# Performance work log

Hardware: AMD Instinct MI355X
Metric: run time of the kernel (lower is better)

## Reference

```python
import jax, jax.numpy as jnp
import numpy as np

B, S, H = 4, 2048, 1024
NUM_HEADS = 16
HEAD_DIM = H // NUM_HEADS


def setup_inputs() -> dict:
    key = jax.random.key(0)
    ks = jax.random.split(key, 11)
    s = 0.02
    return {
        "query": jax.random.normal(ks[0], (B, S, H), dtype=jnp.float32),
        "key_in": jax.random.normal(ks[1], (B, S, H), dtype=jnp.float32),
        "value": jax.random.normal(ks[2], (B, S, H), dtype=jnp.float32),
        "Wq": jax.random.normal(ks[3], (H, H), dtype=jnp.float32) * s,
        "bq": jnp.zeros((H,), dtype=jnp.float32),
        "Wk": jax.random.normal(ks[4], (H, H), dtype=jnp.float32) * s,
        "bk": jnp.zeros((H,), dtype=jnp.float32),
        "Wv": jax.random.normal(ks[5], (HEAD_DIM, H), dtype=jnp.float32) * s,
        "bv": jnp.zeros((HEAD_DIM,), dtype=jnp.float32),
        "Wo": jax.random.normal(ks[6], (H, HEAD_DIM), dtype=jnp.float32) * s,
        "bo": jnp.zeros((H,), dtype=jnp.float32),
    }


def reference(query, key_in, value, Wq, bq, Wk, bk, Wv, bv, Wo, bo):
    scale = HEAD_DIM ** -0.5
    # Linear projections (torch Linear: x @ W.T + b)
    Q = (query @ Wq.T + bq).reshape(B, S, NUM_HEADS, HEAD_DIM).transpose(0, 2, 1, 3)  # [B,h,S,d]
    K = (key_in @ Wk.T + bk).reshape(B, S, NUM_HEADS, HEAD_DIM).transpose(0, 2, 1, 3)  # [B,h,S,d]
    V = value @ Wv.T + bv  # shared single V: [B,S,d]
    attn_scores = jnp.einsum("bhqd,bhkd->bhqk", Q, K) * scale  # [B,h,S,S]
    attn_weights = jax.nn.softmax(attn_scores, axis=-1)
    # dropout is identity at inference
    avg_attn = attn_weights.mean(axis=1)  # head-averaged weights [B,S,S]
    attn_out = jnp.einsum("bqk,bkd->bqd", avg_attn, V)  # [B,S,d]
    output = attn_out @ Wo.T + bo  # [B,S,H]
    return output, avg_attn
```

## Files before the change

kernel.cpp:

```cpp
#include <hip/hip_runtime.h>
#include <hip/hip_bf16.h>


typedef float f32x4 __attribute__((ext_vector_type(4)));
typedef short s16x8 __attribute__((ext_vector_type(8)));

#define DEVI static __device__ __forceinline__
#define MFMA16(a, b, c) __builtin_amdgcn_mfma_f32_16x16x32_bf16(a, b, c, 0, 0, 0)

DEVI unsigned short f2bf(float f) {
  union { float f; unsigned u; } v; v.f = f;
  return (unsigned short)((v.u + 0x7fffu + ((v.u >> 16) & 1u)) >> 16);
}

DEVI s16x8 pack2(f32x4 lo, f32x4 hi) {
  s16x8 r;
  r[0] = (short)f2bf(lo[0]); r[1] = (short)f2bf(lo[1]);
  r[2] = (short)f2bf(lo[2]); r[3] = (short)f2bf(lo[3]);
  r[4] = (short)f2bf(hi[0]); r[5] = (short)f2bf(hi[1]);
  r[6] = (short)f2bf(hi[2]); r[7] = (short)f2bf(hi[3]);
  return r;
}

DEVI float fast_exp2(float x) {
#if __has_builtin(__builtin_amdgcn_exp2f)
  return __builtin_amdgcn_exp2f(x);
#else
  return exp2f(x);
#endif
}

__global__ __launch_bounds__(256, 2) void proj_qk(
    const float* __restrict__ q_in, const float* __restrict__ k_in,
    const float* __restrict__ Wq, const float* __restrict__ Wk,
    const float* __restrict__ bq, const float* __restrict__ bk,
    unsigned short* __restrict__ Qb, unsigned short* __restrict__ Kb) {
  const float* A = blockIdx.z ? k_in : q_in;
  const float* Bw = blockIdx.z ? Wk : Wq;
  const float* bias = blockIdx.z ? bk : bq;
  unsigned short* C = blockIdx.z ? Kb : Qb;

  __shared__ short As[128][32];
  __shared__ short Bs[128][32];

  const int t = threadIdx.x;
  const int lane = t & 63, wid = t >> 6;
  const int wm = wid >> 1, wn = wid & 1;
  const int fr = lane & 15, g = lane >> 4;
  const int m0 = blockIdx.x * 128, n0 = blockIdx.y * 128;

  const int sr = t >> 1, sc = (t & 1) * 16;
  const float* Ap = A + (size_t)(m0 + sr) * 1024 + sc;
  const float* Bp = Bw + (size_t)(n0 + sr) * 1024 + sc;

  f32x4 acc[4][4];
#pragma unroll
  for (int i = 0; i < 4; ++i)
#pragma unroll
    for (int j = 0; j < 4; ++j) acc[i][j] = (f32x4){0.f, 0.f, 0.f, 0.f};

  for (int kt = 0; kt < 32; ++kt) {
    const f32x4 ar0 = *(const f32x4*)(Ap + 0), ar1 = *(const f32x4*)(Ap + 4),
                ar2 = *(const f32x4*)(Ap + 8), ar3 = *(const f32x4*)(Ap + 12);
    const f32x4 br0 = *(const f32x4*)(Bp + 0), br1 = *(const f32x4*)(Bp + 4),
                br2 = *(const f32x4*)(Bp + 8), br3 = *(const f32x4*)(Bp + 12);
    Ap += 32; Bp += 32;
    __syncthreads();
    *(s16x8*)&As[sr][sc] = pack2(ar0, ar1);
    *(s16x8*)&As[sr][sc + 8] = pack2(ar2, ar3);
    *(s16x8*)&Bs[sr][sc] = pack2(br0, br1);
    *(s16x8*)&Bs[sr][sc + 8] = pack2(br2, br3);
    __syncthreads();

    s16x8 af[4], bf[4];
#pragma unroll
    for (int mt = 0; mt < 4; ++mt) af[mt] = *(const s16x8*)&As[wm * 64 + mt * 16 + fr][g * 8];
#pragma unroll
    for (int nt = 0; nt < 4; ++nt) bf[nt] = *(const s16x8*)&Bs[wn * 64 + nt * 16 + fr][g * 8];
#pragma unroll
    for (int mt = 0; mt < 4; ++mt)
#pragma unroll
      for (int nt = 0; nt < 4; ++nt)
        acc[mt][nt] = MFMA16(af[mt], bf[nt], acc[mt][nt]);
  }

#pragma unroll
  for (int nt = 0; nt < 4; ++nt) {
    const int col = n0 + wn * 64 + nt * 16 + fr;
    const float bb = bias[col];
#pragma unroll
    for (int mt = 0; mt < 4; ++mt) {
      const int row = m0 + wm * 64 + mt * 16 + g * 4;
#pragma unroll
      for (int r = 0; r < 4; ++r)
        C[(size_t)(row + r) * 1024 + col] = f2bf(acc[mt][nt][r] + bb);
    }
  }
}

__global__ __launch_bounds__(256, 2) void proj_v(
    const float* __restrict__ val, const float* __restrict__ Wv,
    const float* __restrict__ bv, unsigned short* __restrict__ Vt) {
  __shared__ short As[64][32];
  __shared__ short Bs[64][32];
  const int t = threadIdx.x, lane = t & 63, w = t >> 6;
  const int fr = lane & 15, g = lane >> 4;
  const int m0 = blockIdx.x * 64;
  const int sr = t >> 2, sc = (t & 3) * 8;
  const float* Ap = val + (size_t)(m0 + sr) * 1024 + sc;
  const float* Bp = Wv + (size_t)sr * 1024 + sc;

  f32x4 acc[4];
#pragma unroll
  for (int i = 0; i < 4; ++i) acc[i] = (f32x4){0.f, 0.f, 0.f, 0.f};

  for (int kt = 0; kt < 32; ++kt) {
    const f32x4 a0 = *(const f32x4*)Ap, a1 = *(const f32x4*)(Ap + 4);
    const f32x4 b0 = *(const f32x4*)Bp, b1 = *(const f32x4*)(Bp + 4);
    Ap += 32; Bp += 32;
    __syncthreads();
    *(s16x8*)&As[sr][sc] = pack2(a0, a1);
    *(s16x8*)&Bs[sr][sc] = pack2(b0, b1);
    __syncthreads();
    const s16x8 a = *(const s16x8*)&As[w * 16 + fr][g * 8];
#pragma unroll
    for (int nt = 0; nt < 4; ++nt) {
      const s16x8 b = *(const s16x8*)&Bs[nt * 16 + fr][g * 8];
      acc[nt] = MFMA16(a, b, acc[nt]);
    }
  }
#pragma unroll
  for (int nt = 0; nt < 4; ++nt) {
    const int d = nt * 16 + fr;
    const float bb = bv[d];
#pragma unroll
    for (int r = 0; r < 4; ++r) {
      const int srow = m0 + w * 16 + g * 4 + r;
      Vt[((size_t)(srow >> 11) * 64 + d) * 2048 + (srow & 2047)] = f2bf(acc[nt][r] + bb);
    }
  }
}

__global__ __launch_bounds__(512, 2) void attn_avg(
    const unsigned short* __restrict__ Qb, const unsigned short* __restrict__ Kb,
    float* __restrict__ avg_out) {
  __shared__ short Qs[16 * 1024];
  __shared__ float redm[16][8];
  __shared__ float redl[16][8];

  const int t = threadIdx.x, lane = t & 63, w = t >> 6;
  const int fr = lane & 15, g = lane >> 4;
  int bx = blockIdx.x;
  bx = (bx & 7) * 64 + (bx >> 3);
  const int b = bx >> 7, q0 = (bx & 127) << 4;

  const unsigned short* Qrow = Qb + (size_t)(b * 2048 + q0) * 1024;
#pragma unroll
  for (int j = 0; j < 4; ++j) {
    const int c = t + 512 * j;
    *(s16x8*)(Qs + c * 8) = *(const s16x8*)(Qrow + c * 8);
  }
  __syncthreads();

  float avg[16][4];
#pragma unroll
  for (int kt = 0; kt < 16; ++kt)
#pragma unroll
    for (int r = 0; r < 4; ++r) avg[kt][r] = 0.f;

  const float cs = 0.125f * 1.44269504088896340736f;
  const unsigned short* Kbase = Kb + (size_t)(b * 2048 + w * 256) * 1024;

  for (int h = 0; h < 16; ++h) {
    const s16x8 a0 = *(const s16x8*)&Qs[fr * 1024 + h * 64 + g * 8];
    const s16x8 a1 = *(const s16x8*)&Qs[fr * 1024 + h * 64 + 32 + g * 8];
    float s[16][4];
    float mx[4] = {-3.0e38f, -3.0e38f, -3.0e38f, -3.0e38f};
#pragma unroll
    for (int kt = 0; kt < 16; ++kt) {
      const unsigned short* kp = Kbase + (size_t)(kt * 16 + fr) * 1024 + h * 64 + g * 8;
      const s16x8 b0 = *(const s16x8*)kp;
      const s16x8 b1 = *(const s16x8*)(kp + 32);
      f32x4 sc = (f32x4){0.f, 0.f, 0.f, 0.f};
      sc = MFMA16(a0, b0, sc);
      sc = MFMA16(a1, b1, sc);
#pragma unroll
      for (int r = 0; r < 4; ++r) { s[kt][r] = sc[r]; mx[r] = fmaxf(mx[r], sc[r]); }
    }
#pragma unroll
    for (int d = 1; d < 16; d <<= 1)
#pragma unroll
      for (int r = 0; r < 4; ++r) mx[r] = fmaxf(mx[r], __shfl_xor(mx[r], d));
    if (fr == 0) {
#pragma unroll
      for (int r = 0; r < 4; ++r) redm[g * 4 + r][w] = mx[r];
    }
    __syncthreads();
    float mc[4], lsum[4];
#pragma unroll
    for (int r = 0; r < 4; ++r) {
      const f32x4 p0 = *(const f32x4*)&redm[g * 4 + r][0];
      const f32x4 p1 = *(const f32x4*)&redm[g * 4 + r][4];
      const float m8 = fmaxf(fmaxf(fmaxf(p0[0], p0[1]), fmaxf(p0[2], p0[3])),
                             fmaxf(fmaxf(p1[0], p1[1]), fmaxf(p1[2], p1[3])));
      mc[r] = m8 * cs;
      lsum[r] = 0.f;
    }
#pragma unroll
    for (int kt = 0; kt < 16; ++kt)
#pragma unroll
      for (int r = 0; r < 4; ++r) {
        const float e = fast_exp2(s[kt][r] * cs - mc[r]);
        s[kt][r] = e;
        lsum[r] += e;
      }
#pragma unroll
    for (int d = 1; d < 16; d <<= 1)
#pragma unroll
      for (int r = 0; r < 4; ++r) lsum[r] += __shfl_xor(lsum[r], d);
    if (fr == 0) {
#pragma unroll
      for (int r = 0; r < 4; ++r) redl[g * 4 + r][w] = lsum[r];
    }
    __syncthreads();
    float inv[4];
#pragma unroll
    for (int r = 0; r < 4; ++r) {
      const f32x4 p0 = *(const f32x4*)&redl[g * 4 + r][0];
      const f32x4 p1 = *(const f32x4*)&redl[g * 4 + r][4];
      const float lt = ((p0[0] + p0[1]) + (p0[2] + p0[3])) + ((p1[0] + p1[1]) + (p1[2] + p1[3]));
      inv[r] = 1.0f / (16.0f * lt);
    }
#pragma unroll
    for (int kt = 0; kt < 16; ++kt)
#pragma unroll
      for (int r = 0; r < 4; ++r) avg[kt][r] += s[kt][r] * inv[r];
  }

  float* orow = avg_out + (size_t)(b * 2048 + q0 + g * 4) * 2048 + w * 256 + fr;
#pragma unroll
  for (int kt = 0; kt < 16; ++kt)
#pragma unroll
    for (int r = 0; r < 4; ++r)
      orow[(size_t)r * 2048 + kt * 16] = avg[kt][r];
}

__global__ __launch_bounds__(256, 2) void pv_out(
    const float* __restrict__ avg, const unsigned short* __restrict__ Vt,
    unsigned short* __restrict__ AOb) {
  const int t = threadIdx.x, lane = t & 63, w = t >> 6;
  const int fr = lane & 15, g = lane >> 4;
  const int bx = blockIdx.x;
  const int b = bx >> 5, q0 = (bx & 31) * 64;
  const float* ap = avg + (size_t)(b * 2048 + q0 + w * 16 + fr) * 2048 + g * 8;
  const unsigned short* vp = Vt + ((size_t)b * 64 + fr) * 2048 + g * 8;
  f32x4 acc[4];
#pragma unroll
  for (int i = 0; i < 4; ++i) acc[i] = (f32x4){0.f, 0.f, 0.f, 0.f};
  for (int kt = 0; kt < 64; ++kt) {
    const f32x4 alo = *(const f32x4*)(ap + kt * 32);
    const f32x4 ahi = *(const f32x4*)(ap + kt * 32 + 4);
    const s16x8 a = pack2(alo, ahi);
#pragma unroll
    for (int nt = 0; nt < 4; ++nt) {
      const s16x8 bfr = *(const s16x8*)(vp + (size_t)nt * 16 * 2048 + kt * 32);
      acc[nt] = MFMA16(a, bfr, acc[nt]);
    }
  }
#pragma unroll
  for (int nt = 0; nt < 4; ++nt) {
    const int d = nt * 16 + fr;
#pragma unroll
    for (int r = 0; r < 4; ++r)
      AOb[(size_t)(b * 2048 + q0 + w * 16 + g * 4 + r) * 64 + d] = f2bf(acc[nt][r]);
  }
}

__global__ __launch_bounds__(256, 2) void proj_o(
    const unsigned short* __restrict__ AOb, const float* __restrict__ Wo,
    const float* __restrict__ bo, float* __restrict__ out) {
  const int t = threadIdx.x, lane = t & 63, wid = t >> 6;
  const int wm = wid >> 1, wn = wid & 1;
  const int fr = lane & 15, g = lane >> 4;
  const int m0 = blockIdx.x * 128, n0 = blockIdx.y * 128;
  f32x4 acc[4][4];
#pragma unroll
  for (int i = 0; i < 4; ++i)
#pragma unroll
    for (int j = 0; j < 4; ++j) acc[i][j] = (f32x4){0.f, 0.f, 0.f, 0.f};
#pragma unroll
  for (int ks = 0; ks < 2; ++ks) {
    s16x8 af[4], bf[4];
#pragma unroll
    for (int mt = 0; mt < 4; ++mt)
      af[mt] = *(const s16x8*)(AOb + (size_t)(m0 + wm * 64 + mt * 16 + fr) * 64 + ks * 32 + g * 8);
#pragma unroll
    for (int nt = 0; nt < 4; ++nt) {
      const float* wp = Wo + (size_t)(n0 + wn * 64 + nt * 16 + fr) * 64 + ks * 32 + g * 8;
      bf[nt] = pack2(*(const f32x4*)wp, *(const f32x4*)(wp + 4));
    }
#pragma unroll
    for (int mt = 0; mt < 4; ++mt)
#pragma unroll
      for (int nt = 0; nt < 4; ++nt)
        acc[mt][nt] = MFMA16(af[mt], bf[nt], acc[mt][nt]);
  }
#pragma unroll
  for (int nt = 0; nt < 4; ++nt) {
    const int col = n0 + wn * 64 + nt * 16 + fr;
    const float bb = bo[col];
#pragma unroll
    for (int mt = 0; mt < 4; ++mt) {
      const int row = m0 + wm * 64 + mt * 16 + g * 4;
#pragma unroll
      for (int r = 0; r < 4; ++r)
        out[(size_t)(row + r) * 1024 + col] = acc[mt][nt][r] + bb;
    }
  }
}

extern "C" void kernel_launch(void* const* d_in, const int* in_sizes, int n_in,
                              void* d_out, int out_size, void* d_ws, size_t ws_size,
                              hipStream_t stream) {
  const float* query = (const float*)d_in[0];
  const float* key_in = (const float*)d_in[1];
  const float* value = (const float*)d_in[2];
  const float* Wq = (const float*)d_in[3];
  const float* bq = (const float*)d_in[4];
  const float* Wk = (const float*)d_in[5];
  const float* bk = (const float*)d_in[6];
  const float* Wv = (const float*)d_in[7];
  const float* bv = (const float*)d_in[8];
  const float* Wo = (const float*)d_in[9];
  const float* bo = (const float*)d_in[10];

  unsigned short* Qb = (unsigned short*)d_ws;
  unsigned short* Kb = Qb + 8388608;
  unsigned short* Vt = Kb + 8388608;
  unsigned short* AOb = Vt + 524288;

  float* out = (float*)d_out;
  float* avg_out = out + 8388608;

  hipLaunchKernelGGL(proj_qk, dim3(64, 8, 2), dim3(256), 0, stream,
                     query, key_in, Wq, Wk, bq, bk, Qb, Kb);
  hipLaunchKernelGGL(proj_v, dim3(128), dim3(256), 0, stream, value, Wv, bv, Vt);
  hipLaunchKernelGGL(attn_avg, dim3(512), dim3(512), 0, stream, Qb, Kb, avg_out);
  hipLaunchKernelGGL(pv_out, dim3(128), dim3(256), 0, stream, avg_out, Vt, AOb);
  hipLaunchKernelGGL(proj_o, dim3(64, 8), dim3(256), 0, stream, AOb, Wo, bo, out);
}
```

Measured before the change: 645.8 us.

## Stage K through double-buffered LDS and split attention into two exp passes

A separate kernel now casts the Q/K inputs and weights to bf16. The QK projection then streams 64-wide k-tiles into swizzled, double-buffered LDS using global_load_lds. The softmax scale and log2e are folded into the Q projection output. The head-averaging attention kernel now uses 1024-thread blocks over 32 query rows, staging K tiles asynchronously through LDS. It runs two passes: the first accumulates exp sums per head, the second recomputes the scores and adds normalized probabilities, dropping the max subtraction. This is meant to remove uncoalesced per-wave K loads and the register cost of holding scores, at the price of computing QK^T twice and the risk of exp overflow when scores are large.

```diff
diff --git a/kernel.cpp b/kernel.cpp
--- a/kernel.cpp
+++ b/kernel.cpp
@@ -7,6 +7,9 @@
 
 #define DEVI static __device__ __forceinline__
 #define MFMA16(a, b, c) __builtin_amdgcn_mfma_f32_16x16x32_bf16(a, b, c, 0, 0, 0)
+#define WAITV(N) asm volatile("s_waitcnt vmcnt(" #N ")" ::: "memory")
+#define WAITL()  asm volatile("s_waitcnt lgkmcnt(0)" ::: "memory")
+#define BAR()    __builtin_amdgcn_s_barrier()
 
 DEVI unsigned short f2bf(float f) {
   union { float f; unsigned u; } v; v.f = f;
@@ -30,28 +33,52 @@
 #endif
 }
 
+DEVI void gld16(const void* g, const void* lds) {
+  __builtin_amdgcn_global_load_lds(
+      (const __attribute__((address_space(1))) unsigned int*)g,
+      (__attribute__((address_space(3))) unsigned int*)lds, 16, 0, 0);
+}
+
+__global__ __launch_bounds__(256) void cast_bf16(
+    const float* __restrict__ q, const float* __restrict__ k,
+    const float* __restrict__ Wq, const float* __restrict__ Wk,
+    unsigned short* __restrict__ qbf, unsigned short* __restrict__ kbf,
+    unsigned short* __restrict__ wqb, unsigned short* __restrict__ wkb) {
+  const int bid = blockIdx.x;
+  const float* src; unsigned short* dst; size_t base;
+  if (bid < 1024)      { src = q;  dst = qbf; base = (size_t)bid * 8192; }
+  else if (bid < 2048) { src = k;  dst = kbf; base = (size_t)(bid - 1024) * 8192; }
+  else if (bid < 2176) { src = Wq; dst = wqb; base = (size_t)(bid - 2048) * 8192; }
+  else                 { src = Wk; dst = wkb; base = (size_t)(bid - 2176) * 8192; }
+#pragma unroll
+  for (int j = 0; j < 4; ++j) {
+    const size_t i = base + (size_t)j * 2048 + threadIdx.x * 8;
+    const f32x4 lo = *(const f32x4*)&src[i];
+    const f32x4 hi = *(const f32x4*)&src[i + 4];
+    *(s16x8*)&dst[i] = pack2(lo, hi);
+  }
+}
+
 __global__ __launch_bounds__(256, 2) void proj_qk(
-    const float* __restrict__ q_in, const float* __restrict__ k_in,
-    const float* __restrict__ Wq, const float* __restrict__ Wk,
+    const unsigned short* __restrict__ qbf, const unsigned short* __restrict__ kbf,
+    const unsigned short* __restrict__ wqb, const unsigned short* __restrict__ wkb,
     const float* __restrict__ bq, const float* __restrict__ bk,
     unsigned short* __restrict__ Qb, unsigned short* __restrict__ Kb) {
-  const float* A = blockIdx.z ? k_in : q_in;
-  const float* Bw = blockIdx.z ? Wk : Wq;
+  __shared__ unsigned short As[2][128 * 64];
+  __shared__ unsigned short Bs[2][128 * 64];
+  const unsigned short* A = blockIdx.z ? kbf : qbf;
+  const unsigned short* Bw = blockIdx.z ? wkb : wqb;
   const float* bias = blockIdx.z ? bk : bq;
   unsigned short* C = blockIdx.z ? Kb : Qb;
-
-  __shared__ short As[128][32];
-  __shared__ short Bs[128][32];
-
-  const int t = threadIdx.x;
-  const int lane = t & 63, wid = t >> 6;
-  const int wm = wid >> 1, wn = wid & 1;
+  const float oscale = blockIdx.z ? 1.0f : 0.18033688011112042f;
+
+  const int t = threadIdx.x, lane = t & 63, w = t >> 6;
+  const int wm = w >> 1, wn = w & 1;
   const int fr = lane & 15, g = lane >> 4;
   const int m0 = blockIdx.x * 128, n0 = blockIdx.y * 128;
 
-  const int sr = t >> 1, sc = (t & 1) * 16;
-  const float* Ap = A + (size_t)(m0 + sr) * 1024 + sc;
-  const float* Bp = Bw + (size_t)(n0 + sr) * 1024 + sc;
+  const int srow = w * 32 + (lane >> 3);
+  const int gby = ((lane & 7) << 4);
 
   f32x4 acc[4][4];
 #pragma unroll
@@ -59,29 +86,47 @@
 #pragma unroll
     for (int j = 0; j < 4; ++j) acc[i][j] = (f32x4){0.f, 0.f, 0.f, 0.f};
 
-  for (int kt = 0; kt < 32; ++kt) {
-    const f32x4 ar0 = *(const f32x4*)(Ap + 0), ar1 = *(const f32x4*)(Ap + 4),
-                ar2 = *(const f32x4*)(Ap + 8), ar3 = *(const f32x4*)(Ap + 12);
-    const f32x4 br0 = *(const f32x4*)(Bp + 0), br1 = *(const f32x4*)(Bp + 4),
-                br2 = *(const f32x4*)(Bp + 8), br3 = *(const f32x4*)(Bp + 12);
-    Ap += 32; Bp += 32;
-    __syncthreads();
-    *(s16x8*)&As[sr][sc] = pack2(ar0, ar1);
-    *(s16x8*)&As[sr][sc + 8] = pack2(ar2, ar3);
-    *(s16x8*)&Bs[sr][sc] = pack2(br0, br1);
-    *(s16x8*)&Bs[sr][sc + 8] = pack2(br2, br3);
-    __syncthreads();
-
-    s16x8 af[4], bf[4];
-#pragma unroll
-    for (int mt = 0; mt < 4; ++mt) af[mt] = *(const s16x8*)&As[wm * 64 + mt * 16 + fr][g * 8];
-#pragma unroll
-    for (int nt = 0; nt < 4; ++nt) bf[nt] = *(const s16x8*)&Bs[wn * 64 + nt * 16 + fr][g * 8];
-#pragma unroll
-    for (int mt = 0; mt < 4; ++mt)
-#pragma unroll
-      for (int nt = 0; nt < 4; ++nt)
-        acc[mt][nt] = MFMA16(af[mt], bf[nt], acc[mt][nt]);
+#define PSTAGE(ks)                                                          \
+  {                                                                         \
+    const int _buf = (ks) & 1;                                              \
+    _Pragma("unroll") for (int j = 0; j < 4; ++j) {                         \
+      const int row = srow + j * 8;                                         \
+      const int gb = gby ^ ((row & 7) << 4);                                \
+      gld16(A + (size_t)(m0 + row) * 1024 + (ks) * 64 + (gb >> 1),          \
+            &As[_buf][w * 2048 + j * 512]);                                 \
+      gld16(Bw + (size_t)(n0 + row) * 1024 + (ks) * 64 + (gb >> 1),         \
+            &Bs[_buf][w * 2048 + j * 512]);                                 \
+    }                                                                       \
+  }
+
+  PSTAGE(0);
+  for (int ks = 0; ks < 16; ++ks) {
+    WAITL(); BAR();
+    if (ks < 15) { PSTAGE(ks + 1); WAITV(8); } else { WAITV(0); }
+    __builtin_amdgcn_sched_barrier(0);
+    const unsigned short* Ab = As[ks & 1];
+    const unsigned short* Bb = Bs[ks & 1];
+    s16x8 af[2][4], bf[2][4];
+#pragma unroll
+    for (int k = 0; k < 2; ++k) {
+#pragma unroll
+      for (int mt = 0; mt < 4; ++mt) {
+        const int row = wm * 64 + mt * 16 + fr;
+        af[k][mt] = *(const s16x8*)&Ab[row * 64 + (((k * 64 + g * 16) ^ ((row & 7) << 4)) >> 1)];
+      }
+#pragma unroll
+      for (int nt = 0; nt < 4; ++nt) {
+        const int row = wn * 64 + nt * 16 + fr;
+        bf[k][nt] = *(const s16x8*)&Bb[row * 64 + (((k * 64 + g * 16) ^ ((row & 7) << 4)) >> 1)];
+      }
+    }
+#pragma unroll
+    for (int k = 0; k < 2; ++k)
+#pragma unroll
+      for (int mt = 0; mt < 4; ++mt)
+#pragma unroll
+        for (int nt = 0; nt < 4; ++nt)
+          acc[mt][nt] = MFMA16(af[k][mt], bf[k][nt], acc[mt][nt]);
   }
 
 #pragma unroll
@@ -93,16 +138,17 @@
       const int row = m0 + wm * 64 + mt * 16 + g * 4;
 #pragma unroll
       for (int r = 0; r < 4; ++r)
-        C[(size_t)(row + r) * 1024 + col] = f2bf(acc[mt][nt][r] + bb);
-    }
-  }
+        C[(size_t)(row + r) * 1024 + col] = f2bf((acc[mt][nt][r] + bb) * oscale);
+    }
+  }
+#undef PSTAGE
 }
 
 __global__ __launch_bounds__(256, 2) void proj_v(
     const float* __restrict__ val, const float* __restrict__ Wv,
     const float* __restrict__ bv, unsigned short* __restrict__ Vt) {
-  __shared__ short As[64][32];
-  __shared__ short Bs[64][32];
+  __shared__ short As2[64][32];
+  __shared__ short Bs2[64][32];
   const int t = threadIdx.x, lane = t & 63, w = t >> 6;
   const int fr = lane & 15, g = lane >> 4;
   const int m0 = blockIdx.x * 64;
@@ -119,13 +165,13 @@
     const f32x4 b0 = *(const f32x4*)Bp, b1 = *(const f32x4*)(Bp + 4);
     Ap += 32; Bp += 32;
     __syncthreads();
-    *(s16x8*)&As[sr][sc] = pack2(a0, a1);
-    *(s16x8*)&Bs[sr][sc] = pack2(b0, b1);
+    *(s16x8*)&As2[sr][sc] = pack2(a0, a1);
+    *(s16x8*)&Bs2[sr][sc] = pack2(b0, b1);
     __syncthreads();
-    const s16x8 a = *(const s16x8*)&As[w * 16 + fr][g * 8];
+    const s16x8 a = *(const s16x8*)&As2[w * 16 + fr][g * 8];
 #pragma unroll
     for (int nt = 0; nt < 4; ++nt) {
-      const s16x8 b = *(const s16x8*)&Bs[nt * 16 + fr][g * 8];
+      const s16x8 b = *(const s16x8*)&Bs2[nt * 16 + fr][g * 8];
       acc[nt] = MFMA16(a, b, acc[nt]);
     }
   }
@@ -135,32 +181,50 @@
     const float bb = bv[d];
 #pragma unroll
     for (int r = 0; r < 4; ++r) {
-      const int srow = m0 + w * 16 + g * 4 + r;
-      Vt[((size_t)(srow >> 11) * 64 + d) * 2048 + (srow & 2047)] = f2bf(acc[nt][r] + bb);
-    }
-  }
-}
-
-__global__ __launch_bounds__(512, 2) void attn_avg(
+      const int srw = m0 + w * 16 + g * 4 + r;
+      Vt[((size_t)(srw >> 11) * 64 + d) * 2048 + (srw & 2047)] = f2bf(acc[nt][r] + bb);
+    }
+  }
+}
+
+__global__ __launch_bounds__(1024, 4) void attn_avg(
     const unsigned short* __restrict__ Qb, const unsigned short* __restrict__ Kb,
     float* __restrict__ avg_out) {
-  __shared__ short Qs[16 * 1024];
-  __shared__ float redm[16][8];
-  __shared__ float redl[16][8];
+  __shared__ unsigned short Qs[32 * 1032];
+  __shared__ unsigned short Ks[2][256 * 64];
+  __shared__ float sums[16][32][8];
 
   const int t = threadIdx.x, lane = t & 63, w = t >> 6;
   const int fr = lane & 15, g = lane >> 4;
+  const int qh = w >> 3, kw = w & 7;
   int bx = blockIdx.x;
-  bx = (bx & 7) * 64 + (bx >> 3);
-  const int b = bx >> 7, q0 = (bx & 127) << 4;
-
-  const unsigned short* Qrow = Qb + (size_t)(b * 2048 + q0) * 1024;
-#pragma unroll
-  for (int j = 0; j < 4; ++j) {
-    const int c = t + 512 * j;
-    *(s16x8*)(Qs + c * 8) = *(const s16x8*)(Qrow + c * 8);
-  }
-  __syncthreads();
+  bx = (bx & 7) * 32 + (bx >> 3);
+  const int b = bx >> 6, q0 = (bx & 63) * 32;
+
+  {
+    const unsigned short* Qg = Qb + (size_t)(b * 2048 + q0) * 1024;
+#pragma unroll
+    for (int j = 0; j < 4; ++j) {
+      const int idx = j * 1024 + t;
+      const int row = idx >> 7, col = (idx & 127) << 3;
+      *(s16x8*)&Qs[row * 1032 + col] = *(const s16x8*)&Qg[(size_t)row * 1024 + col];
+    }
+  }
+
+  const int srow = w * 16 + (lane >> 3);
+  const int gby = (lane & 7) << 4;
+
+#define ASTAGE(s)                                                            \
+  {                                                                          \
+    const int _h = ((s) >> 3) & 15, _ktp = (s) & 7, _buf = (s) & 1;          \
+    _Pragma("unroll") for (int j = 0; j < 2; ++j) {                          \
+      const int row = srow + j * 8;                                          \
+      const int key = (b << 11) + ((row >> 5) << 8) + (_ktp << 5) + (row & 31); \
+      const int gb = gby ^ ((row & 7) << 4);                                 \
+      gld16(Kb + (size_t)key * 1024 + _h * 64 + (gb >> 1),                   \
+            &Ks[_buf][w * 1024 + j * 512]);                                  \
+    }                                                                        \
+  }
 
   float avg[16][4];
 #pragma unroll
@@ -168,81 +232,91 @@
 #pragma unroll
     for (int r = 0; r < 4; ++r) avg[kt][r] = 0.f;
 
-  const float cs = 0.125f * 1.44269504088896340736f;
-  const unsigned short* Kbase = Kb + (size_t)(b * 2048 + w * 256) * 1024;
+  s16x8 aQ0, aQ1;
+  float lsum[4], inv[4];
+
+  ASTAGE(0);
 
   for (int h = 0; h < 16; ++h) {
-    const s16x8 a0 = *(const s16x8*)&Qs[fr * 1024 + h * 64 + g * 8];
-    const s16x8 a1 = *(const s16x8*)&Qs[fr * 1024 + h * 64 + 32 + g * 8];
-    float s[16][4];
-    float mx[4] = {-3.0e38f, -3.0e38f, -3.0e38f, -3.0e38f};
-#pragma unroll
-    for (int kt = 0; kt < 16; ++kt) {
-      const unsigned short* kp = Kbase + (size_t)(kt * 16 + fr) * 1024 + h * 64 + g * 8;
-      const s16x8 b0 = *(const s16x8*)kp;
-      const s16x8 b1 = *(const s16x8*)(kp + 32);
-      f32x4 sc = (f32x4){0.f, 0.f, 0.f, 0.f};
-      sc = MFMA16(a0, b0, sc);
-      sc = MFMA16(a1, b1, sc);
-#pragma unroll
-      for (int r = 0; r < 4; ++r) { s[kt][r] = sc[r]; mx[r] = fmaxf(mx[r], sc[r]); }
-    }
-#pragma unroll
-    for (int d = 1; d < 16; d <<= 1)
-#pragma unroll
-      for (int r = 0; r < 4; ++r) mx[r] = fmaxf(mx[r], __shfl_xor(mx[r], d));
-    if (fr == 0) {
-#pragma unroll
-      for (int r = 0; r < 4; ++r) redm[g * 4 + r][w] = mx[r];
-    }
-    __syncthreads();
-    float mc[4], lsum[4];
-#pragma unroll
-    for (int r = 0; r < 4; ++r) {
-      const f32x4 p0 = *(const f32x4*)&redm[g * 4 + r][0];
-      const f32x4 p1 = *(const f32x4*)&redm[g * 4 + r][4];
-      const float m8 = fmaxf(fmaxf(fmaxf(p0[0], p0[1]), fmaxf(p0[2], p0[3])),
-                             fmaxf(fmaxf(p1[0], p1[1]), fmaxf(p1[2], p1[3])));
-      mc[r] = m8 * cs;
-      lsum[r] = 0.f;
-    }
-#pragma unroll
-    for (int kt = 0; kt < 16; ++kt)
-#pragma unroll
-      for (int r = 0; r < 4; ++r) {
-        const float e = fast_exp2(s[kt][r] * cs - mc[r]);
-        s[kt][r] = e;
-        lsum[r] += e;
-      }
+#pragma unroll
+    for (int r = 0; r < 4; ++r) lsum[r] = 0.f;
+#pragma unroll
+    for (int ktp = 0; ktp < 8; ++ktp) {
+      const int s = h * 8 + ktp;
+      WAITL(); BAR();
+      ASTAGE(s + 1);
+      WAITV(2);
+      __builtin_amdgcn_sched_barrier(0);
+      if (ktp == 0) {
+        aQ0 = *(const s16x8*)&Qs[(qh * 16 + fr) * 1032 + h * 64 + g * 8];
+        aQ1 = *(const s16x8*)&Qs[(qh * 16 + fr) * 1032 + h * 64 + 32 + g * 8];
+      }
+      const unsigned short* Kbuf = Ks[s & 1];
+      const int sw = (fr & 7) << 4;
+#pragma unroll
+      for (int ktsub = 0; ktsub < 2; ++ktsub) {
+        const int row = kw * 32 + ktsub * 16 + fr;
+        const s16x8 b0 = *(const s16x8*)&Kbuf[row * 64 + (((g * 16) ^ sw) >> 1)];
+        const s16x8 b1 = *(const s16x8*)&Kbuf[row * 64 + (((64 + g * 16) ^ sw) >> 1)];
+        f32x4 scv = (f32x4){0.f, 0.f, 0.f, 0.f};
+        scv = MFMA16(aQ0, b0, scv);
+        scv = MFMA16(aQ1, b1, scv);
+#pragma unroll
+        for (int r = 0; r < 4; ++r) lsum[r] += fast_exp2(scv[r]);
+      }
+    }
 #pragma unroll
     for (int d = 1; d < 16; d <<= 1)
 #pragma unroll
       for (int r = 0; r < 4; ++r) lsum[r] += __shfl_xor(lsum[r], d);
     if (fr == 0) {
 #pragma unroll
-      for (int r = 0; r < 4; ++r) redl[g * 4 + r][w] = lsum[r];
-    }
-    __syncthreads();
-    float inv[4];
-#pragma unroll
-    for (int r = 0; r < 4; ++r) {
-      const f32x4 p0 = *(const f32x4*)&redl[g * 4 + r][0];
-      const f32x4 p1 = *(const f32x4*)&redl[g * 4 + r][4];
-      const float lt = ((p0[0] + p0[1]) + (p0[2] + p0[3])) + ((p1[0] + p1[1]) + (p1[2] + p1[3]));
-      inv[r] = 1.0f / (16.0f * lt);
-    }
-#pragma unroll
-    for (int kt = 0; kt < 16; ++kt)
-#pragma unroll
-      for (int r = 0; r < 4; ++r) avg[kt][r] += s[kt][r] * inv[r];
-  }
-
-  float* orow = avg_out + (size_t)(b * 2048 + q0 + g * 4) * 2048 + w * 256 + fr;
+      for (int r = 0; r < 4; ++r) sums[h][qh * 16 + g * 4 + r][kw] = lsum[r];
+    }
+  }
+
+  for (int h = 0; h < 16; ++h) {
+#pragma unroll
+    for (int ktp = 0; ktp < 8; ++ktp) {
+      const int s = 128 + h * 8 + ktp;
+      WAITL(); BAR();
+      if (s < 255) { ASTAGE(s + 1); WAITV(2); } else { WAITV(0); }
+      __builtin_amdgcn_sched_barrier(0);
+      if (ktp == 0) {
+        aQ0 = *(const s16x8*)&Qs[(qh * 16 + fr) * 1032 + h * 64 + g * 8];
+        aQ1 = *(const s16x8*)&Qs[(qh * 16 + fr) * 1032 + h * 64 + 32 + g * 8];
+#pragma unroll
+        for (int r = 0; r < 4; ++r) {
+          const f32x4 s0 = *(const f32x4*)&sums[h][qh * 16 + g * 4 + r][0];
+          const f32x4 s1 = *(const f32x4*)&sums[h][qh * 16 + g * 4 + r][4];
+          inv[r] = 1.0f / (16.0f * (((s0[0] + s0[1]) + (s0[2] + s0[3])) +
+                                    ((s1[0] + s1[1]) + (s1[2] + s1[3]))));
+        }
+      }
+      const unsigned short* Kbuf = Ks[s & 1];
+      const int sw = (fr & 7) << 4;
+#pragma unroll
+      for (int ktsub = 0; ktsub < 2; ++ktsub) {
+        const int row = kw * 32 + ktsub * 16 + fr;
+        const s16x8 b0 = *(const s16x8*)&Kbuf[row * 64 + (((g * 16) ^ sw) >> 1)];
+        const s16x8 b1 = *(const s16x8*)&Kbuf[row * 64 + (((64 + g * 16) ^ sw) >> 1)];
+        f32x4 scv = (f32x4){0.f, 0.f, 0.f, 0.f};
+        scv = MFMA16(aQ0, b0, scv);
+        scv = MFMA16(aQ1, b1, scv);
+#pragma unroll
+        for (int r = 0; r < 4; ++r)
+          avg[ktp * 2 + ktsub][r] += fast_exp2(scv[r]) * inv[r];
+      }
+    }
+  }
+
+  float* orow = avg_out + (size_t)(b * 2048 + q0 + qh * 16 + g * 4) * 2048 + kw * 256 + fr;
 #pragma unroll
   for (int kt = 0; kt < 16; ++kt)
 #pragma unroll
     for (int r = 0; r < 4; ++r)
       orow[(size_t)r * 2048 + kt * 16] = avg[kt][r];
+#undef ASTAGE
 }
 
 __global__ __launch_bounds__(256, 2) void pv_out(
@@ -342,10 +416,17 @@
   float* out = (float*)d_out;
   float* avg_out = out + 8388608;
 
+  unsigned short* qbf = (unsigned short*)avg_out;
+  unsigned short* kbf = qbf + 8388608;
+  unsigned short* wqb = kbf + 8388608;
+  unsigned short* wkb = wqb + 1048576;
+
+  hipLaunchKernelGGL(cast_bf16, dim3(2304), dim3(256), 0, stream,
+                     query, key_in, Wq, Wk, qbf, kbf, wqb, wkb);
   hipLaunchKernelGGL(proj_qk, dim3(64, 8, 2), dim3(256), 0, stream,
-                     query, key_in, Wq, Wk, bq, bk, Qb, Kb);
+                     qbf, kbf, wqb, wkb, bq, bk, Qb, Kb);
   hipLaunchKernelGGL(proj_v, dim3(128), dim3(256), 0, stream, value, Wv, bv, Vt);
-  hipLaunchKernelGGL(attn_avg, dim3(512), dim3(512), 0, stream, Qb, Kb, avg_out);
+  hipLaunchKernelGGL(attn_avg, dim3(256), dim3(1024), 0, stream, Qb, Kb, avg_out);
   hipLaunchKernelGGL(pv_out, dim3(128), dim3(256), 0, stream, avg_out, Vt, AOb);
   hipLaunchKernelGGL(proj_o, dim3(64, 8), dim3(256), 0, stream, AOb, Wo, bo, out);
 }
```

Result: slower. 784.5 us (+21.5%).
